# Optimization experiments

Hardware: AMD Instinct MI355X
Metric: run time of the kernel (lower is better)

The kernel has to match this reference:

```python
import jax, jax.numpy as jnp
import numpy as np

B, L, H, V, HALF = 128, 4096, 64, 64, 32
ALPHA = 0.95
LN_EPS = 1e-5


def _normalize(x):
    # torch F.normalize(dim=-1): x / max(||x||_2, 1e-12)
    n = jnp.linalg.norm(x, axis=-1, keepdims=True)
    return x / jnp.maximum(n, 1e-12)


def setup_inputs() -> dict:
    key = jax.random.key(0)
    ks = jax.random.split(key, 17)
    s = 0.05
    return {
        "seq": jax.random.randint(ks[0], (B, L), 0, V),
        "embed": jax.random.normal(ks[1], (V, H), jnp.float32),
        "W1": jax.random.normal(ks[2], (H, 2 * H), jnp.float32) * s,
        "b1": jnp.zeros((2 * H,), jnp.float32),
        "W2": jax.random.normal(ks[3], (2 * H, H), jnp.float32) * s,
        "b2": jnp.zeros((H,), jnp.float32),
        "gamma": jnp.ones((H,), jnp.float32),
        "beta": jnp.zeros((H,), jnp.float32),
        "Ws": jax.random.normal(ks[4], (H, HALF), jnp.float32) * s,
        "bs": jnp.zeros((HALF,), jnp.float32),
        "We": jax.random.normal(ks[5], (H, HALF), jnp.float32) * s,
        "be": jnp.zeros((HALF,), jnp.float32),
        "Wrp": jax.random.normal(ks[6], (2 * HALF, H), jnp.float32) * s,
        "brp": jnp.zeros((H,), jnp.float32),
        "Wout": jax.random.normal(ks[7], (H, V), jnp.float32) * s,
        "bout": jnp.zeros((V,), jnp.float32),
    }


def _forward(seq, embed, W1, b1, W2, b2, gamma, beta,
             Ws, bs, We, be, Wrp, brp, Wout, bout):
    # Encoder: embed + FF(ReLU) residual + LayerNorm
    h0 = embed[seq]                                   # [B,L,H]
    ff = jnp.maximum(h0 @ W1 + b1, 0.0) @ W2 + b2
    x = h0 + ff
    mu = x.mean(-1, keepdims=True)
    var = ((x - mu) ** 2).mean(-1, keepdims=True)
    h = (x - mu) / jnp.sqrt(var + LN_EPS) * gamma + beta  # [B,L,H]

    # Precompute per-step projections for t = 0 .. L-2
    hp = h[:, :-1, :]                                 # [B,L-1,H]
    hs = hp @ Ws + bs                                 # [B,L-1,HALF]
    he = hp @ We + be
    ksn = _normalize(hs)
    ken = _normalize(he)
    scale = (jnp.arange(L - 1, dtype=h.dtype) + 1.0) / L  # (t+1)/L

    def step(carry, inp):
        M_s, M_e = carry                              # [B,HALF,HALF]
        hs_t, he_t, ks_t, ke_t, sc = inp
        vps = jnp.einsum('bij,bj->bi', M_s, ks_t)
        vpe = jnp.einsum('bij,bj->bi', M_e, ke_t)
        M_s = M_s + (1.0 - ALPHA) * (hs_t - vps)[:, :, None] * ks_t[:, None, :]
        M_e = M_e + (1.0 - ALPHA) * sc * (he_t - vpe)[:, :, None] * ke_t[:, None, :]
        return (M_s, M_e), None

    xs = (jnp.swapaxes(hs, 0, 1), jnp.swapaxes(he, 0, 1),
          jnp.swapaxes(ksn, 0, 1), jnp.swapaxes(ken, 0, 1), scale)
    M0 = jnp.zeros((B, HALF, HALF), h.dtype)
    (M_s, M_e), _ = jax.lax.scan(step, (M0, M0), xs)

    # Read with last-token query
    q = h[:, -1, :]
    qs = _normalize(q @ Ws + bs)
    qe = _normalize(q @ We + be)
    rs = jnp.einsum('bij,bj->bi', M_s, qs)
    re = jnp.einsum('bij,bj->bi', M_e, qe)
    r = jnp.concatenate([rs, re], axis=-1)            # [B,2*HALF]
    return (r @ Wrp + brp) @ Wout + bout              # [B,V]


def reference(seq, embed, W1, b1, W2, b2, gamma, beta,
              Ws, bs, We, be, Wrp, brp, Wout, bout):
    return _forward(seq, embed, W1, b1, W2, b2, gamma, beta,
                    Ws, bs, We, be, Wrp, brp, Wout, bout)
```

## Files before the change

### kernel.cpp

```cpp
#include <hip/hip_runtime.h>
#include <hip/hip_bf16.h>
#include <stdint.h>


#define BETA 0.05f
#define NB 128
#define NL 4096

struct Ptrs { const void* p[15]; };

__device__ inline float readlane_f(float v, int l) {
    return __int_as_float(__builtin_amdgcn_readlane(__float_as_int(v), l));
}
__device__ inline float ldT(const float* p, int i) { return p[i]; }
__device__ inline float ldT(const __hip_bfloat16* p, int i) { return __bfloat162float(p[i]); }

template <typename T>
__device__ void build_tables_body(const T* emb, const T* W1, const T* b1,
                                  const T* W2, const T* b2, const T* gam,
                                  const T* bet, const T* Wsm, const T* bsv,
                                  const T* Wem, const T* bev, float* tbl)
{
    int v = blockIdx.x;
    int j = threadIdx.x;
    __shared__ float h0s[64];
    __shared__ float act[128];
    __shared__ float hrow[64];

    float h0 = ldT(emb, v * 64 + j);
    h0s[j] = h0;
    __syncthreads();

    float za = ldT(b1, j);
    float zb = ldT(b1, j + 64);
    for (int k = 0; k < 64; ++k) {
        float hk = h0s[k];
        za = fmaf(hk, ldT(W1, k * 128 + j), za);
        zb = fmaf(hk, ldT(W1, k * 128 + j + 64), zb);
    }
    act[j] = fmaxf(za, 0.0f);
    act[j + 64] = fmaxf(zb, 0.0f);
    __syncthreads();

    float ff = ldT(b2, j);
    for (int k = 0; k < 128; ++k)
        ff = fmaf(act[k], ldT(W2, k * 64 + j), ff);
    float x = h0 + ff;

    float s = x;
    for (int off = 32; off >= 1; off >>= 1) s += __shfl_xor(s, off, 64);
    float mu = s * (1.0f / 64.0f);
    float d = x - mu;
    float s2 = d * d;
    for (int off = 32; off >= 1; off >>= 1) s2 += __shfl_xor(s2, off, 64);
    float var = s2 * (1.0f / 64.0f);
    float h = d / sqrtf(var + 1e-5f) * ldT(gam, j) + ldT(bet, j);
    hrow[j] = h;
    __syncthreads();

    if (j < 32) {
        float sv = ldT(bsv, j);
        for (int k = 0; k < 64; ++k)
            sv = fmaf(hrow[k], ldT(Wsm, k * 32 + j), sv);
        float n2 = sv * sv;
        for (int off = 16; off >= 1; off >>= 1) n2 += __shfl_xor(n2, off, 64);
        float nrm = fmaxf(sqrtf(n2), 1e-12f);
        tbl[v * 32 + j] = sv;
        tbl[2048 + v * 32 + j] = sv / nrm;
    } else {
        int jj = j - 32;
        float ev = ldT(bev, jj);
        for (int k = 0; k < 64; ++k)
            ev = fmaf(hrow[k], ldT(Wem, k * 32 + jj), ev);
        float n2 = ev * ev;
        for (int off = 16; off >= 1; off >>= 1) n2 += __shfl_xor(n2, off, 64);
        float nrm = fmaxf(sqrtf(n2), 1e-12f);
        tbl[4096 + v * 32 + jj] = ev;
        tbl[6144 + v * 32 + jj] = ev / nrm;
    }
}

__global__ __launch_bounds__(64, 2) void build_tables(Ptrs ps, float* __restrict__ tbl)
{
    uint32_t g0 = *(const uint32_t*)ps.p[5];
    if (g0 == 0x3F803F80u)
        build_tables_body((const __hip_bfloat16*)ps.p[0], (const __hip_bfloat16*)ps.p[1],
                          (const __hip_bfloat16*)ps.p[2], (const __hip_bfloat16*)ps.p[3],
                          (const __hip_bfloat16*)ps.p[4], (const __hip_bfloat16*)ps.p[5],
                          (const __hip_bfloat16*)ps.p[6], (const __hip_bfloat16*)ps.p[7],
                          (const __hip_bfloat16*)ps.p[8], (const __hip_bfloat16*)ps.p[9],
                          (const __hip_bfloat16*)ps.p[10], tbl);
    else
        build_tables_body((const float*)ps.p[0], (const float*)ps.p[1],
                          (const float*)ps.p[2], (const float*)ps.p[3],
                          (const float*)ps.p[4], (const float*)ps.p[5],
                          (const float*)ps.p[6], (const float*)ps.p[7],
                          (const float*)ps.p[8], (const float*)ps.p[9],
                          (const float*)ps.p[10], tbl);
}

template <int MAT>
__device__ inline float mk_tf(int g, int lane) {
    int t1 = g * 64 + lane + 1;
    float f = MAT ? (float)t1 : 1.0f;
    return (t1 == NL) ? 0.0f : f;
}

#define LOADG16(dst, slo, tokv, tfv)                                    \
    { _Pragma("unroll")                                                 \
      for (int j_ = 0; j_ < 16; ++j_) {                                 \
          int rv_ = __builtin_amdgcn_readlane((tokv), (slo) + j_);      \
          float gv_ = GlM[rv_ * 64 + lane];                             \
          if (MAT) gv_ *= readlane_f((tfv), (slo) + j_);                \
          (dst)[j_] = gv_;                                              \
      } }

#define CHAIN16(buf, shi, slo, tokv)                                    \
    { _Pragma("unroll")                                                 \
      for (int jj_ = 0; jj_ < 16; ++jj_) {                              \
          int s_ = (shi) - jj_;                                         \
          int svt_ = __builtin_amdgcn_readlane((tokv), s_);             \
          float sy_ = readlane_f(y, svt_);                              \
          y = fmaf(sy_, (buf)[s_ - (slo)], y);                          \
          csave = (lane == s_) ? sy_ : csave;                           \
      } }

template <int MAT>
__device__ void scan_loop(const int* __restrict__ sb, const float* GlM,
                          float* da, float y, int lane, float bfac)
{
    float csave = 0.0f;
    float g0[16], g1[16];
    int tokc = sb[63 * 64 + lane];
    float tfc = mk_tf<MAT>(63, lane);
    LOADG16(g0, 48, tokc, tfc)
    if (!MAT) g0[15] = 0.0f;
    asm volatile("" ::: "memory");

#pragma unroll 1
    for (int g = 63; g >= 0; --g) {
        int tokn = 0; float tfn = 0.0f;
        if (g > 0) { tokn = sb[(g - 1) * 64 + lane]; tfn = mk_tf<MAT>(g - 1, lane); }
        LOADG16(g1, 32, tokc, tfc)
        asm volatile("" ::: "memory");
        CHAIN16(g0, 63, 48, tokc)
        LOADG16(g0, 16, tokc, tfc)
        asm volatile("" ::: "memory");
        CHAIN16(g1, 47, 32, tokc)
        LOADG16(g1, 0, tokc, tfc)
        asm volatile("" ::: "memory");
        CHAIN16(g0, 31, 16, tokc)
        if (g > 0) { LOADG16(g0, 48, tokn, tfn) }
        asm volatile("" ::: "memory");
        CHAIN16(g1, 15, 0, tokc)
        float dv = csave * (bfac * tfc);
        atomicAdd(&da[tokc], dv);
        tokc = tokn; tfc = tfn;
    }
}

__global__ __launch_bounds__(128, 1) void ema_scan_fused(
    const int* __restrict__ seq, const float* __restrict__ tbl,
    Ptrs ps, void* __restrict__ outv)
{
    __shared__ float Gl[2 * 4096];
    __shared__ float K[2 * 64 * 36];
    __shared__ float daL[128];
    __shared__ float rv[64];
    __shared__ float o1s[64];

    int b = blockIdx.x;
    int tid = threadIdx.x;
    int mat = tid >> 6;
    int lane = tid & 63;

    daL[tid] = 0.0f;

    const float4* ksrc = (const float4*)(tbl + 2048 + mat * 4096);
    float* Km = K + mat * 64 * 36;
    for (int i = lane; i < 512; i += 64) {
        float4 kv = ksrc[i];
        int vv = i >> 3, j = (i & 7) * 4;
        float* kd = Km + vv * 36 + j;
        kd[0] = kv.x; kd[1] = kv.y; kd[2] = kv.z; kd[3] = kv.w;
    }

    float Kown[32];
    {
        const float4* kr = (const float4*)(Km + lane * 36);
#pragma unroll
        for (int j = 0; j < 8; ++j) {
            float4 t = kr[j];
            Kown[4 * j + 0] = t.x; Kown[4 * j + 1] = t.y;
            Kown[4 * j + 2] = t.z; Kown[4 * j + 3] = t.w;
        }
    }

    const int* sb = seq + (size_t)b * NL;
    int vlast = sb[NL - 1];
    float bfac = mat ? (BETA / 4096.0f) : BETA;
    float* GlM = Gl + mat * 4096;

    float y = 0.0f;
#pragma unroll 2
    for (int vt = 0; vt < 64; ++vt) {
        const float4* rr = (const float4*)(Km + vt * 36);
        float acc = 0.0f;
#pragma unroll
        for (int j = 0; j < 8; ++j) {
            float4 t = rr[j];
            acc = fmaf(t.x, Kown[4 * j + 0], acc);
            acc = fmaf(t.y, Kown[4 * j + 1], acc);
            acc = fmaf(t.z, Kown[4 * j + 2], acc);
            acc = fmaf(t.w, Kown[4 * j + 3], acc);
        }
        GlM[vt * 64 + lane] = acc * (-bfac);
        if (vt == vlast) y = acc;
    }

    if (mat == 0) scan_loop<0>(sb, GlM, daL, y, lane, BETA);
    else          scan_loop<1>(sb, GlM, daL + 64, y, lane, BETA / 4096.0f);

    __syncthreads();

    if (tid < 64) {
        int half = tid >> 5;
        int j = tid & 31;
        const float* hsrc = tbl + half * 4096;
        const float* dv = daL + half * 64;
        float r = 0.0f;
        for (int v = 0; v < 64; ++v)
            r = fmaf(dv[v], hsrc[v * 32 + j], r);
        rv[tid] = r;
    }
    __syncthreads();

    uint32_t g0h = *(const uint32_t*)ps.p[5];
    int isbf = (g0h == 0x3F803F80u) ? 1 : 0;
    if (tid < 64) {
        float o;
        if (isbf) {
            const __hip_bfloat16* W = (const __hip_bfloat16*)ps.p[11];
            o = __bfloat162float(((const __hip_bfloat16*)ps.p[12])[tid]);
            for (int i = 0; i < 64; ++i)
                o = fmaf(rv[i], __bfloat162float(W[i * 64 + tid]), o);
        } else {
            const float* W = (const float*)ps.p[11];
            o = ((const float*)ps.p[12])[tid];
            for (int i = 0; i < 64; ++i)
                o = fmaf(rv[i], W[i * 64 + tid], o);
        }
        o1s[tid] = o;
    }
    __syncthreads();
    if (tid < 64) {
        float o2;
        if (isbf) {
            const __hip_bfloat16* W = (const __hip_bfloat16*)ps.p[13];
            o2 = __bfloat162float(((const __hip_bfloat16*)ps.p[14])[tid]);
            for (int i = 0; i < 64; ++i)
                o2 = fmaf(o1s[i], __bfloat162float(W[i * 64 + tid]), o2);
            ((__hip_bfloat16*)outv)[b * 64 + tid] = __float2bfloat16(o2);
        } else {
            const float* W = (const float*)ps.p[13];
            o2 = ((const float*)ps.p[14])[tid];
            for (int i = 0; i < 64; ++i)
                o2 = fmaf(o1s[i], W[i * 64 + tid], o2);
            ((float*)outv)[b * 64 + tid] = o2;
        }
    }
}

extern "C" void kernel_launch(void* const* d_in, const int* in_sizes, int n_in,
                              void* d_out, int out_size, void* d_ws, size_t ws_size,
                              hipStream_t stream) {
    const int* seq = (const int*)d_in[0];
    Ptrs ps;
    for (int i = 0; i < 15; ++i) ps.p[i] = d_in[i + 1];

    float* tbl = (float*)d_ws;

    build_tables<<<64, 64, 0, stream>>>(ps, tbl);
    ema_scan_fused<<<NB, 128, 0, stream>>>(seq, tbl, ps, d_out);
}
```

Measured before the change: 225.0 us.

## Block the serial scan chain into 4-step groups using bpermute-gathered coefficients

Replaces the per-step serial dependency chain (a readlane on y followed by an FMA for each of 64 steps) with groups of four steps. Each group's scalar values are solved from a small triangular system whose coefficients are gathered through ds_bpermute. A permuted copy ry is kept and updated alongside y, which shortens the serial readlane dependency per group. The cost is extra bpermute, readlane and FMA work per step, more register use, and no longer prefetching the next group's loads across iterations.

```diff
diff --git a/kernel.cpp b/kernel.cpp
--- a/kernel.cpp
+++ b/kernel.cpp
@@ -11,6 +11,9 @@
 
 __device__ inline float readlane_f(float v, int l) {
     return __int_as_float(__builtin_amdgcn_readlane(__float_as_int(v), l));
+}
+__device__ inline float bperm_f(int idx, float v) {
+    return __int_as_float(__builtin_amdgcn_ds_bpermute(idx, __float_as_int(v)));
 }
 __device__ inline float ldT(const float* p, int i) { return p[i]; }
 __device__ inline float ldT(const __hip_bfloat16* p, int i) { return __bfloat162float(p[i]); }
@@ -106,53 +109,93 @@
     return (t1 == NL) ? 0.0f : f;
 }
 
-#define LOADG16(dst, slo, tokv, tfv)                                    \
-    { _Pragma("unroll")                                                 \
-      for (int j_ = 0; j_ < 16; ++j_) {                                 \
-          int rv_ = __builtin_amdgcn_readlane((tokv), (slo) + j_);      \
-          float gv_ = GlM[rv_ * 64 + lane];                             \
-          if (MAT) gv_ *= readlane_f((tfv), (slo) + j_);                \
-          (dst)[j_] = gv_;                                              \
-      } }
-
-#define CHAIN16(buf, shi, slo, tokv)                                    \
-    { _Pragma("unroll")                                                 \
-      for (int jj_ = 0; jj_ < 16; ++jj_) {                              \
-          int s_ = (shi) - jj_;                                         \
-          int svt_ = __builtin_amdgcn_readlane((tokv), s_);             \
-          float sy_ = readlane_f(y, svt_);                              \
-          y = fmaf(sy_, (buf)[s_ - (slo)], y);                          \
-          csave = (lane == s_) ? sy_ : csave;                           \
-      } }
+#define LOAD4(P, K)                                                        \
+    {                                                                      \
+        const int La_ = 63 - 4 * (K);                                      \
+        int va_ = __builtin_amdgcn_readlane(tokc, La_);                    \
+        int vb_ = __builtin_amdgcn_readlane(tokc, La_ - 1);                \
+        int vc_ = __builtin_amdgcn_readlane(tokc, La_ - 2);                \
+        int vd_ = __builtin_amdgcn_readlane(tokc, La_ - 3);                \
+        float a_ = GlM[va_ * 64 + lane];                                   \
+        float b_ = GlM[vb_ * 64 + lane];                                   \
+        float c_ = GlM[vc_ * 64 + lane];                                   \
+        float d_ = GlM[vd_ * 64 + lane];                                   \
+        if (MAT) {                                                         \
+            a_ *= readlane_f(tfc, La_);                                    \
+            b_ *= readlane_f(tfc, La_ - 1);                                \
+            c_ *= readlane_f(tfc, La_ - 2);                                \
+            d_ *= readlane_f(tfc, La_ - 3);                                \
+        }                                                                  \
+        if (!MAT && (K) == 0 && g == 63) a_ = 0.0f;       \
+        gv[P][0] = a_; gv[P][1] = b_; gv[P][2] = c_; gv[P][3] = d_;        \
+        gt[P][0] = bperm_f(idx, a_);                                       \
+        gt[P][1] = bperm_f(idx, b_);                                       \
+        gt[P][2] = bperm_f(idx, c_);                                       \
+        gt[P][3] = bperm_f(idx, d_);                                       \
+        c01[P] = readlane_f(gt[P][0], La_ - 1);                            \
+        c02[P] = readlane_f(gt[P][0], La_ - 2);                            \
+        c03[P] = readlane_f(gt[P][0], La_ - 3);                            \
+        c12[P] = readlane_f(gt[P][1], La_ - 2);                            \
+        c13[P] = readlane_f(gt[P][1], La_ - 3);                            \
+        c23[P] = readlane_f(gt[P][2], La_ - 3);                            \
+    }
+
+#define CHAIN4(P, K)                                                       \
+    {                                                                      \
+        const int La_ = 63 - 4 * (K);                                      \
+        float ra_ = readlane_f(ry, La_);                                   \
+        float rb_ = readlane_f(ry, La_ - 1);                               \
+        float rc_ = readlane_f(ry, La_ - 2);                               \
+        float rd_ = readlane_f(ry, La_ - 3);                               \
+        float sA_ = ra_;                                                   \
+        float sB_ = fmaf(sA_, c01[P], rb_);                                \
+        float sC_ = fmaf(sB_, c12[P], fmaf(sA_, c02[P], rc_));             \
+        float sD_ = fmaf(sC_, c23[P], fmaf(sB_, c13[P],                    \
+                          fmaf(sA_, c03[P], rd_)));                        \
+        ry = fmaf(sA_, gt[P][0], ry);                                      \
+        ry = fmaf(sB_, gt[P][1], ry);                                      \
+        ry = fmaf(sC_, gt[P][2], ry);                                      \
+        ry = fmaf(sD_, gt[P][3], ry);                                      \
+        y = fmaf(sA_, gv[P][0], y);                                        \
+        y = fmaf(sB_, gv[P][1], y);                                        \
+        y = fmaf(sC_, gv[P][2], y);                                        \
+        y = fmaf(sD_, gv[P][3], y);                                        \
+        csave = (lane == La_) ? sA_ : csave;                               \
+        csave = (lane == La_ - 1) ? sB_ : csave;                           \
+        csave = (lane == La_ - 2) ? sC_ : csave;                           \
+        csave = (lane == La_ - 3) ? sD_ : csave;                           \
+    }
 
 template <int MAT>
 __device__ void scan_loop(const int* __restrict__ sb, const float* GlM,
                           float* da, float y, int lane, float bfac)
 {
     float csave = 0.0f;
-    float g0[16], g1[16];
     int tokc = sb[63 * 64 + lane];
     float tfc = mk_tf<MAT>(63, lane);
-    LOADG16(g0, 48, tokc, tfc)
-    if (!MAT) g0[15] = 0.0f;
-    asm volatile("" ::: "memory");
 
 #pragma unroll 1
     for (int g = 63; g >= 0; --g) {
         int tokn = 0; float tfn = 0.0f;
         if (g > 0) { tokn = sb[(g - 1) * 64 + lane]; tfn = mk_tf<MAT>(g - 1, lane); }
-        LOADG16(g1, 32, tokc, tfc)
-        asm volatile("" ::: "memory");
-        CHAIN16(g0, 63, 48, tokc)
-        LOADG16(g0, 16, tokc, tfc)
-        asm volatile("" ::: "memory");
-        CHAIN16(g1, 47, 32, tokc)
-        LOADG16(g1, 0, tokc, tfc)
-        asm volatile("" ::: "memory");
-        CHAIN16(g0, 31, 16, tokc)
-        if (g > 0) { LOADG16(g0, 48, tokn, tfn) }
-        asm volatile("" ::: "memory");
-        CHAIN16(g1, 15, 0, tokc)
+        int idx = tokc << 2;
+        float ry = bperm_f(idx, y);
+
+        float gv[2][4], gt[2][4];
+        float c01[2], c02[2], c03[2], c12[2], c13[2], c23[2];
+
+        LOAD4(0, 0)
+#pragma unroll
+        for (int k = 0; k < 16; ++k) {
+            if (k < 15) {
+                if ((k & 1) == 0) LOAD4(1, k + 1)
+                else              LOAD4(0, k + 1)
+            }
+            asm volatile("" ::: "memory");
+            if ((k & 1) == 0) CHAIN4(0, k)
+            else              CHAIN4(1, k)
+        }
+
         float dv = csave * (bfac * tfc);
         atomicAdd(&da[tokc], dv);
         tokc = tokn; tfc = tfn;
```

New measurement: 349.7 us. +55.4%, slower.

## Split scan into chunked producer/consumer warps with per-matrix blocks

Applied to the files above, without the earlier changes.

Replaces the single-wave sequential reverse scan per matrix with a chunked scheme. Each batch/matrix pair now gets its own 512-thread block, seven producer waves precompute 32x32 chunk transfer matrices in parallel, and one consumer wave applies them in double-buffered LDS slots. A cross-block atomic flag lets the second finishing block of each batch run the output projection. This is meant to shorten the serial dependency chain and use more CUs, at the cost of extra triangular-solve arithmetic, block syncs each round, and a global-atomic handoff.

```diff
diff --git a/kernel.cpp b/kernel.cpp
--- a/kernel.cpp
+++ b/kernel.cpp
@@ -6,11 +6,25 @@
 #define BETA 0.05f
 #define NB 128
 #define NL 4096
+#define TC 32
+#define NCH 128
+#define SLOT_F 1088
+#define NSLOT 14
+
+#define L_GR   (NSLOT * SLOT_F)
+#define L_DA   (L_GR + 4096)
+#define L_RV   (L_DA + 64)
+#define L_O1   (L_RV + 64)
+#define L_WHO  (L_O1 + 64)
+#define L_TOT  (L_WHO + 4)
 
 struct Ptrs { const void* p[15]; };
 
 __device__ inline float readlane_f(float v, int l) {
     return __int_as_float(__builtin_amdgcn_readlane(__float_as_int(v), l));
+}
+__device__ inline float bperm_f(int idx, float v) {
+    return __int_as_float(__builtin_amdgcn_ds_bpermute(idx, __float_as_int(v)));
 }
 __device__ inline float ldT(const float* p, int i) { return p[i]; }
 __device__ inline float ldT(const __hip_bfloat16* p, int i) { return __bfloat162float(p[i]); }
@@ -80,8 +94,13 @@
     }
 }
 
-__global__ __launch_bounds__(64, 2) void build_tables(Ptrs ps, float* __restrict__ tbl)
+__global__ __launch_bounds__(64, 2) void build_tables(Ptrs ps, float* __restrict__ tbl,
+                                                      int* __restrict__ flags)
 {
+    if (blockIdx.x == 0) {
+        flags[threadIdx.x] = 0;
+        flags[threadIdx.x + 64] = 0;
+    }
     uint32_t g0 = *(const uint32_t*)ps.p[5];
     if (g0 == 0x3F803F80u)
         build_tables_body((const __hip_bfloat16*)ps.p[0], (const __hip_bfloat16*)ps.p[1],
@@ -99,140 +118,154 @@
                           (const float*)ps.p[10], tbl);
 }
 
-template <int MAT>
-__device__ inline float mk_tf(int g, int lane) {
-    int t1 = g * 64 + lane + 1;
-    float f = MAT ? (float)t1 : 1.0f;
-    return (t1 == NL) ? 0.0f : f;
-}
-
-#define LOADG16(dst, slo, tokv, tfv)                                    \
-    { _Pragma("unroll")                                                 \
-      for (int j_ = 0; j_ < 16; ++j_) {                                 \
-          int rv_ = __builtin_amdgcn_readlane((tokv), (slo) + j_);      \
-          float gv_ = GlM[rv_ * 64 + lane];                             \
-          if (MAT) gv_ *= readlane_f((tfv), (slo) + j_);                \
-          (dst)[j_] = gv_;                                              \
-      } }
-
-#define CHAIN16(buf, shi, slo, tokv)                                    \
-    { _Pragma("unroll")                                                 \
-      for (int jj_ = 0; jj_ < 16; ++jj_) {                              \
-          int s_ = (shi) - jj_;                                         \
-          int svt_ = __builtin_amdgcn_readlane((tokv), s_);             \
-          float sy_ = readlane_f(y, svt_);                              \
-          y = fmaf(sy_, (buf)[s_ - (slo)], y);                          \
-          csave = (lane == s_) ? sy_ : csave;                           \
-      } }
-
-template <int MAT>
-__device__ void scan_loop(const int* __restrict__ sb, const float* GlM,
-                          float* da, float y, int lane, float bfac)
+__global__ __launch_bounds__(512, 1) void ema_ms(
+    const int* __restrict__ seq, const float* __restrict__ tbl,
+    Ptrs ps, float* __restrict__ rvbuf, int* __restrict__ flags,
+    void* __restrict__ outv)
 {
-    float csave = 0.0f;
-    float g0[16], g1[16];
-    int tokc = sb[63 * 64 + lane];
-    float tfc = mk_tf<MAT>(63, lane);
-    LOADG16(g0, 48, tokc, tfc)
-    if (!MAT) g0[15] = 0.0f;
-    asm volatile("" ::: "memory");
-
-#pragma unroll 1
-    for (int g = 63; g >= 0; --g) {
-        int tokn = 0; float tfn = 0.0f;
-        if (g > 0) { tokn = sb[(g - 1) * 64 + lane]; tfn = mk_tf<MAT>(g - 1, lane); }
-        LOADG16(g1, 32, tokc, tfc)
-        asm volatile("" ::: "memory");
-        CHAIN16(g0, 63, 48, tokc)
-        LOADG16(g0, 16, tokc, tfc)
-        asm volatile("" ::: "memory");
-        CHAIN16(g1, 47, 32, tokc)
-        LOADG16(g1, 0, tokc, tfc)
-        asm volatile("" ::: "memory");
-        CHAIN16(g0, 31, 16, tokc)
-        if (g > 0) { LOADG16(g0, 48, tokn, tfn) }
-        asm volatile("" ::: "memory");
-        CHAIN16(g1, 15, 0, tokc)
-        float dv = csave * (bfac * tfc);
-        atomicAdd(&da[tokc], dv);
-        tokc = tokn; tfc = tfn;
-    }
-}
-
-__global__ __launch_bounds__(128, 1) void ema_scan_fused(
-    const int* __restrict__ seq, const float* __restrict__ tbl,
-    Ptrs ps, void* __restrict__ outv)
-{
-    __shared__ float Gl[2 * 4096];
-    __shared__ float K[2 * 64 * 36];
-    __shared__ float daL[128];
-    __shared__ float rv[64];
-    __shared__ float o1s[64];
-
-    int b = blockIdx.x;
+    __shared__ float S[L_TOT];
+
+    int bm = blockIdx.x;
+    int b = bm >> 1, mat = bm & 1;
     int tid = threadIdx.x;
-    int mat = tid >> 6;
-    int lane = tid & 63;
-
-    daL[tid] = 0.0f;
-
-    const float4* ksrc = (const float4*)(tbl + 2048 + mat * 4096);
-    float* Km = K + mat * 64 * 36;
-    for (int i = lane; i < 512; i += 64) {
-        float4 kv = ksrc[i];
-        int vv = i >> 3, j = (i & 7) * 4;
-        float* kd = Km + vv * 36 + j;
-        kd[0] = kv.x; kd[1] = kv.y; kd[2] = kv.z; kd[3] = kv.w;
-    }
-
-    float Kown[32];
+    int wid = tid >> 6, lane = tid & 63;
+    const float bstep = BETA / 4096.0f;
+
+    if (tid < 64) S[L_DA + tid] = 0.0f;
+
+    const float* ktab = tbl + 2048 + mat * 4096;
+    for (int i = tid; i < 2048; i += 512)
+        S[(i >> 5) * 33 + (i & 31)] = ktab[i];
+    __syncthreads();
+
     {
-        const float4* kr = (const float4*)(Km + lane * 36);
-#pragma unroll
-        for (int j = 0; j < 8; ++j) {
-            float4 t = kr[j];
-            Kown[4 * j + 0] = t.x; Kown[4 * j + 1] = t.y;
-            Kown[4 * j + 2] = t.z; Kown[4 * j + 3] = t.w;
+        float Kown[32];
+#pragma unroll
+        for (int j = 0; j < 32; ++j) Kown[j] = S[lane * 33 + j];
+        for (int v8 = 0; v8 < 8; ++v8) {
+            int vt = wid * 8 + v8;
+            float acc = 0.0f;
+#pragma unroll
+            for (int j = 0; j < 32; ++j)
+                acc = fmaf(S[vt * 33 + j], Kown[j], acc);
+            S[L_GR + vt * 64 + lane] = acc;
         }
     }
+    __syncthreads();
 
     const int* sb = seq + (size_t)b * NL;
-    int vlast = sb[NL - 1];
-    float bfac = mat ? (BETA / 4096.0f) : BETA;
-    float* GlM = Gl + mat * 4096;
-
     float y = 0.0f;
-#pragma unroll 2
-    for (int vt = 0; vt < 64; ++vt) {
-        const float4* rr = (const float4*)(Km + vt * 36);
-        float acc = 0.0f;
-#pragma unroll
-        for (int j = 0; j < 8; ++j) {
-            float4 t = rr[j];
-            acc = fmaf(t.x, Kown[4 * j + 0], acc);
-            acc = fmaf(t.y, Kown[4 * j + 1], acc);
-            acc = fmaf(t.z, Kown[4 * j + 2], acc);
-            acc = fmaf(t.w, Kown[4 * j + 3], acc);
+    if (wid == 0) {
+        int vlast = sb[NL - 1];
+        y = S[L_GR + vlast * 64 + lane];
+    }
+
+    for (int r = 0; r <= 19; ++r) {
+        if (wid >= 1) {
+            int ci = 7 * r + (wid - 1);
+            if (r <= 18 && ci < NCH) {
+                int c = NCH - 1 - ci;
+                float* slot = S + ((r & 1) * 7 + (wid - 1)) * SLOT_F;
+                int t = c * TC + 31 - lane;
+                int tok = 0; float bneg = 0.0f;
+                if (lane < 32) {
+                    tok = sb[t];
+                    float bb = mat ? bstep * (float)(t + 1) : BETA;
+                    if (t == NL - 1) bb = 0.0f;
+                    bneg = -bb;
+                    ((int*)(slot + 1056))[lane] = tok;
+                }
+                float grow[32];
+#pragma unroll
+                for (int p = 0; p < 32; ++p) {
+                    int vp = __builtin_amdgcn_readlane(tok, p);
+                    grow[p] = S[L_GR + vp * 64 + tok] * bneg;
+                }
+                float x[32];
+                x[0] = (lane == 0) ? 1.0f : 0.0f;
+#pragma unroll
+                for (int p = 1; p < 32; ++p) {
+                    float xp = (lane == p) ? 1.0f : 0.0f;
+#pragma unroll
+                    for (int j = 0; j < p; ++j)
+                        xp = fmaf(readlane_f(grow[p], j), x[j], xp);
+                    x[p] = xp;
+                }
+                if (lane < 32) {
+#pragma unroll
+                    for (int p = 0; p < 32; ++p)
+                        slot[p * 33 + lane] = x[p];
+                }
+            }
+        } else {
+            if (r >= 1) {
+                for (int w2 = 0; w2 < 7; ++w2) {
+                    int ci = 7 * (r - 1) + w2;
+                    if (ci >= NCH) break;
+                    int c = NCH - 1 - ci;
+                    float* slot = S + (((r - 1) & 1) * 7 + w2) * SLOT_F;
+                    int tokf = (lane < 32) ? ((int*)(slot + 1056))[lane] : 0;
+                    int t = c * TC + 31 - lane;
+                    float bv = 0.0f;
+                    if (lane < 32) {
+                        float bb = mat ? bstep * (float)(t + 1) : BETA;
+                        if (t == NL - 1) bb = 0.0f;
+                        bv = bb;
+                    }
+                    float ry = bperm_f(tokf << 2, y);
+                    float vrow[32];
+#pragma unroll
+                    for (int q = 0; q < 32; ++q)
+                        vrow[q] = slot[(lane & 31) * 33 + q];
+                    float growf[32];
+#pragma unroll
+                    for (int p = 0; p < 32; ++p) {
+                        int vp = __builtin_amdgcn_readlane(tokf, p);
+                        growf[p] = S[L_GR + vp * 64 + lane];
+                    }
+                    float s0 = 0.f, s1 = 0.f, s2 = 0.f, s3 = 0.f;
+#pragma unroll
+                    for (int q = 0; q < 32; q += 4) {
+                        s0 = fmaf(vrow[q + 0], readlane_f(ry, q + 0), s0);
+                        s1 = fmaf(vrow[q + 1], readlane_f(ry, q + 1), s1);
+                        s2 = fmaf(vrow[q + 2], readlane_f(ry, q + 2), s2);
+                        s3 = fmaf(vrow[q + 3], readlane_f(ry, q + 3), s3);
+                    }
+                    float dv = ((s0 + s1) + (s2 + s3)) * bv;
+                    if (lane < 32) atomicAdd(&S[L_DA + tokf], dv);
+                    float ya = 0.0f, yb = 0.0f;
+#pragma unroll
+                    for (int p = 0; p < 32; p += 2) {
+                        ya = fmaf(-readlane_f(dv, p), growf[p], ya);
+                        yb = fmaf(-readlane_f(dv, p + 1), growf[p + 1], yb);
+                    }
+                    y += ya + yb;
+                }
+            }
         }
-        GlM[vt * 64 + lane] = acc * (-bfac);
-        if (vt == vlast) y = acc;
-    }
-
-    if (mat == 0) scan_loop<0>(sb, GlM, daL, y, lane, BETA);
-    else          scan_loop<1>(sb, GlM, daL + 64, y, lane, BETA / 4096.0f);
-
-    __syncthreads();
-
-    if (tid < 64) {
-        int half = tid >> 5;
-        int j = tid & 31;
-        const float* hsrc = tbl + half * 4096;
-        const float* dv = daL + half * 64;
-        float r = 0.0f;
+        __syncthreads();
+    }
+
+    if (tid < 32) {
+        float rr = 0.0f;
+        const float* hsrc = tbl + mat * 4096;
         for (int v = 0; v < 64; ++v)
-            r = fmaf(dv[v], hsrc[v * 32 + j], r);
-        rv[tid] = r;
-    }
+            rr = fmaf(S[L_DA + v], hsrc[v * 32 + tid], rr);
+        __hip_atomic_store(&rvbuf[bm * 32 + tid], rr,
+                           __ATOMIC_RELAXED, __HIP_MEMORY_SCOPE_AGENT);
+    }
+    __syncthreads();
+    if (tid == 0) {
+        int old = __hip_atomic_fetch_add(&flags[b], 1,
+                                         __ATOMIC_ACQ_REL, __HIP_MEMORY_SCOPE_AGENT);
+        ((int*)S)[L_WHO] = old;
+    }
+    __syncthreads();
+    if (((int*)S)[L_WHO] != 1) return;
+
+    if (tid < 64)
+        S[L_RV + tid] = __hip_atomic_load(&rvbuf[b * 64 + tid],
+                                          __ATOMIC_RELAXED, __HIP_MEMORY_SCOPE_AGENT);
     __syncthreads();
 
     uint32_t g0h = *(const uint32_t*)ps.p[5];
@@ -243,14 +276,14 @@
             const __hip_bfloat16* W = (const __hip_bfloat16*)ps.p[11];
             o = __bfloat162float(((const __hip_bfloat16*)ps.p[12])[tid]);
             for (int i = 0; i < 64; ++i)
-                o = fmaf(rv[i], __bfloat162float(W[i * 64 + tid]), o);
+                o = fmaf(S[L_RV + i], __bfloat162float(W[i * 64 + tid]), o);
         } else {
             const float* W = (const float*)ps.p[11];
             o = ((const float*)ps.p[12])[tid];
             for (int i = 0; i < 64; ++i)
-                o = fmaf(rv[i], W[i * 64 + tid], o);
+                o = fmaf(S[L_RV + i], W[i * 64 + tid], o);
         }
-        o1s[tid] = o;
+        S[L_O1 + tid] = o;
     }
     __syncthreads();
     if (tid < 64) {
@@ -259,13 +292,13 @@
             const __hip_bfloat16* W = (const __hip_bfloat16*)ps.p[13];
             o2 = __bfloat162float(((const __hip_bfloat16*)ps.p[14])[tid]);
             for (int i = 0; i < 64; ++i)
-                o2 = fmaf(o1s[i], __bfloat162float(W[i * 64 + tid]), o2);
+                o2 = fmaf(S[L_O1 + i], __bfloat162float(W[i * 64 + tid]), o2);
             ((__hip_bfloat16*)outv)[b * 64 + tid] = __float2bfloat16(o2);
         } else {
             const float* W = (const float*)ps.p[13];
             o2 = ((const float*)ps.p[14])[tid];
             for (int i = 0; i < 64; ++i)
-                o2 = fmaf(o1s[i], W[i * 64 + tid], o2);
+                o2 = fmaf(S[L_O1 + i], W[i * 64 + tid], o2);
             ((float*)outv)[b * 64 + tid] = o2;
         }
     }
@@ -279,7 +312,9 @@
     for (int i = 0; i < 15; ++i) ps.p[i] = d_in[i + 1];
 
     float* tbl = (float*)d_ws;
-
-    build_tables<<<64, 64, 0, stream>>>(ps, tbl);
-    ema_scan_fused<<<NB, 128, 0, stream>>>(seq, tbl, ps, d_out);
-}
+    float* rvbuf = tbl + 8192;
+    int* flags = (int*)(rvbuf + 8192);
+
+    build_tables<<<64, 64, 0, stream>>>(ps, tbl, flags);
+    ema_ms<<<NB * 2, 512, 0, stream>>>(seq, tbl, ps, rvbuf, flags, d_out);
+}
```

After: 245.0 us. +8.9%, slower.
